# Performance work log

Hardware: AMD Instinct MI355X
Metric: run time of the kernel (lower is better)

## Reference

```python
import jax, jax.numpy as jnp
import numpy as np

EPS_SINK = 0.01   # SinkhornDistance eps
N_ITERS = 20      # fixed iteration count (original: max 100 with host-side early exit)
BN_EPS = 1e-5


def _conv(x, w, b):
    # NCHW 3x3 (or 1x1) conv, SAME padding
    y = jax.lax.conv_general_dilated(x, w, (1, 1), 'SAME',
                                     dimension_numbers=('NCHW', 'OIHW', 'NCHW'))
    return y + b[None, :, None, None]


def _bn_train(x, gamma, beta):
    # BatchNorm2d in training mode: batch statistics over (N,H,W)
    m = jnp.mean(x, axis=(0, 2, 3), keepdims=True)
    v = jnp.var(x, axis=(0, 2, 3), keepdims=True)
    return gamma[None, :, None, None] * (x - m) * jax.lax.rsqrt(v + BN_EPS) + beta[None, :, None, None]


def _calc_mean_std(f, eps=1e-5):
    m = jnp.mean(f, axis=(2, 3), keepdims=True)
    s = jnp.sqrt(jnp.var(f, axis=(2, 3), keepdims=True) + eps)
    return m, s


def _sinkhorn_pi(x, y, eps):
    # x: [b, n, d] content points, y: [b, m, d] style points. Cosine-distance cost.
    xn = x / jnp.linalg.norm(x, axis=-1, keepdims=True)
    yn = y / jnp.linalg.norm(y, axis=-1, keepdims=True)
    C = 1.0 - jnp.einsum('bnd,bmd->bnm', xn, yn)          # [b, n, m]
    b, n, m = C.shape
    log_mu = jnp.log(jnp.full((b, n), 1.0 / n) + 1e-8)
    log_nu = jnp.log(jnp.full((b, m), 1.0 / m) + 1e-8)

    def Mmat(u, v):
        # (-C + u_i + v_j) / eps
        return (-C + u[..., None] + v[..., None, :]) / eps

    def step(carry, _):
        u, v = carry
        u = eps * (log_mu - jax.scipy.special.logsumexp(Mmat(u, v), axis=-1)) + u
        v = eps * (log_nu - jax.scipy.special.logsumexp(Mmat(u, v), axis=-2)) + v
        return (u, v), None

    (u, v), _ = jax.lax.scan(step, (jnp.zeros((b, n)), jnp.zeros((b, m))), None, length=N_ITERS)
    return jnp.exp(Mmat(u, v))                             # transport plan pi


def setup_inputs() -> dict:
    key = jax.random.key(0)
    ks = jax.random.split(key, 16)
    bs, dim, h, w = 4, 512, 32, 32
    s = 0.05
    return {
        'content_feat': jax.random.normal(ks[0], (bs, dim, h, w), jnp.float32),
        'style_feat':   jax.random.normal(ks[1], (bs, dim, h, w), jnp.float32),
        # alpha_predictor (version 1): conv(1024->256,3x3) ReLU BN, conv(256->256,3x3) ReLU BN, conv(256->512,3x3)
        'w1': jax.random.normal(ks[2], (256, 1024, 3, 3), jnp.float32) * s,
        'b1': jnp.zeros((256,), jnp.float32),
        'g1': jnp.ones((256,), jnp.float32),
        'be1': jnp.zeros((256,), jnp.float32),
        'w2': jax.random.normal(ks[3], (256, 256, 3, 3), jnp.float32) * s,
        'b2': jnp.zeros((256,), jnp.float32),
        'g2': jnp.ones((256,), jnp.float32),
        'be2': jnp.zeros((256,), jnp.float32),
        'w3': jax.random.normal(ks[4], (512, 256, 3, 3), jnp.float32) * s,
        'b3': jnp.zeros((512,), jnp.float32),
        # stand-in decoder head: 3x3 conv 512->3 (decoder is an external injected module)
        'dec_w': jax.random.normal(ks[5], (3, 512, 3, 3), jnp.float32) * s,
        'dec_b': jnp.zeros((3,), jnp.float32),
    }


def reference(content_feat, style_feat, w1, b1, g1, be1, w2, b2, g2, be2, w3, b3, dec_w, dec_b):
    bs, dim, h, w = content_feat.shape
    cf = content_feat.reshape(bs, dim, h * w).transpose(0, 2, 1)   # [b, hw, d]
    sf = style_feat.reshape(bs, dim, h * w).transpose(0, 2, 1)
    pi = _sinkhorn_pi(cf, sf, EPS_SINK) * (h * w)                  # style_assign: pi * h * w
    t = jnp.einsum('bnm,bmd->bnd', pi, sf).transpose(0, 2, 1).reshape(bs, dim, h, w)
    cm, cs = _calc_mean_std(content_feat)
    c_normed = (content_feat - cm) / cs
    a = _bn_train(jax.nn.relu(_conv(jnp.concatenate([t, content_feat], axis=1), w1, b1)), g1, be1)
    a = _bn_train(jax.nn.relu(_conv(a, w2, b2)), g2, be2)
    alpha = _conv(a, w3, b3)
    t = alpha * c_normed + t
    g_t = _conv(t, dec_w, dec_b)
    return g_t
```

## Files before the change

### kernel.cpp

```cpp
#include <hip/hip_runtime.h>

typedef unsigned short u16;
typedef unsigned int u32;
typedef float f32x4 __attribute__((ext_vector_type(4)));
typedef short bf16x8 __attribute__((ext_vector_type(8)));

#define DEV static __device__ __forceinline__

DEV float bf2f(u16 u){ union{float f; u32 i;} x; x.i = ((u32)u) << 16; return x.f; }
DEV u16 f2bf(float f){ union{float f; u32 i;} x; x.f = f; u32 u = x.i;
  return (u16)((u + 0x7fffu + ((u >> 16) & 1u)) >> 16); }
DEV u16 f2h(float f){ _Float16 h = (_Float16)f; u16 u; __builtin_memcpy(&u, &h, 2); return u; }
DEV float h2f(u16 u){ _Float16 h; __builtin_memcpy(&h, &u, 2); return (float)h; }
DEV uint4 pack8(const u16* s){ uint4 v;
  v.x = (u32)s[0] | ((u32)s[1]<<16); v.y = (u32)s[2] | ((u32)s[3]<<16);
  v.z = (u32)s[4] | ((u32)s[5]<<16); v.w = (u32)s[6] | ((u32)s[7]<<16); return v; }
DEV f32x4 mfma16(bf16x8 a, bf16x8 b, f32x4 c){
  return __builtin_amdgcn_mfma_f32_16x16x32_bf16(a, b, c, 0, 0, 0);
}
DEV bf16x8 ldfrag(const u16* p){ return *(const bf16x8*)p; }

constexpr float SCL = 144.269504088896341f;
constexpr float LOG2MU = -9.99998522680257f;

constexpr size_t MB = 1ull << 20;
constexpr size_t OFF_G    = 0;
constexpr size_t OFF_GT   = 8*MB;
constexpr size_t OFF_U    = 16*MB;
constexpr size_t OFF_V    = OFF_U   + (16<<10);
constexpr size_t OFF_INC  = OFF_V   + (16<<10);
constexpr size_t OFF_INS  = OFF_INC + (16<<10);
constexpr size_t OFF_CNM  = OFF_INS + (16<<10);
constexpr size_t OFF_CNIS = OFF_CNM + (8<<10);
constexpr size_t OFF_BNS  = OFF_CNIS+ (8<<10);
constexpr size_t OFF_PNP  = OFF_BNS + (4<<10);
constexpr size_t OFF_CFH  = 17*MB;
constexpr size_t OFF_CFL  = 21*MB;
constexpr size_t OFF_SFH  = 25*MB;
constexpr size_t OFF_SFL  = 29*MB;
constexpr size_t OFF_SNB  = 33*MB;
constexpr size_t OFF_TN   = 37*MB;
constexpr size_t OFF_TCP  = 45*MB;
constexpr size_t OFF_W1P  = 53*MB;
constexpr size_t OFF_W2P  = OFF_W1P + 9*256*1024*2;
constexpr size_t OFF_W3P  = OFF_W2P + 9*256*256*2;
constexpr size_t OFF_WDP  = OFF_W3P + 9*512*256*2;
constexpr size_t OFF_PIP  = 62*MB;
constexpr size_t OFF_Z1  = 17*MB;
constexpr size_t OFF_A1P = 25*MB;
constexpr size_t OFF_Z2  = 27*MB;
constexpr size_t OFF_A2P = 35*MB;
constexpr size_t OFF_T2P = 17*MB;

DEV void pack_one(const float* __restrict__ w, u16* __restrict__ wp, int CO, int CI, int o){
  int e = o & 7;
  int lane = (o >> 3) & 63;
  int t2 = o >> 9;
  int tap = t2 % 9;
  int r3 = t2 / 9;
  int NCK = CI >> 5;
  int ck = r3 % NCK;
  int g  = r3 / NCK;
  int co = g*16 + (lane & 15);
  int ci = ck*32 + ((lane >> 4) & 3)*8 + e;
  wp[o] = f2bf(w[(size_t)(co*CI + ci)*9 + tap]);
}

constexpr int NW1 = 9*256*1024, NW2 = 9*256*256, NW3 = 9*512*256, NWD = 9*16*512;
__global__ void pack_all_k(const float* __restrict__ w1, const float* __restrict__ w2,
                           const float* __restrict__ w3, const float* __restrict__ wd,
                           u16* __restrict__ w1p, u16* __restrict__ w2p,
                           u16* __restrict__ w3p, u16* __restrict__ wdp){
  int o = blockIdx.x*256 + threadIdx.x;
  if (o < NW1){ pack_one(w1, w1p, 256, 1024, o); return; }
  o -= NW1;
  if (o < NW2){ pack_one(w2, w2p, 256, 256, o); return; }
  o -= NW2;
  if (o < NW3){ pack_one(w3, w3p, 512, 256, o); return; }
  o -= NW3;
  if (o < NWD){
    int ci = o & 511; int r = o >> 9; int co = r & 15; int tap = r >> 4;
    wdp[o] = f2bf((co < 3) ? wd[(size_t)(co*512 + ci)*9 + tap] : 0.f);
  }
}

__global__ void pix_part_k(const float* __restrict__ cf, const float* __restrict__ sf,
                           float* __restrict__ part){
  int src = blockIdx.z;
  const float* in = src ? sf : cf;
  int p = blockIdx.x*256 + threadIdx.x;
  int b = p >> 10, pp = p & 1023;
  int d0 = blockIdx.y*64;
  const float* base = in + ((size_t)(b*512 + d0))*1024 + pp;
  float s = 0.f;
  #pragma unroll 8
  for (int d = 0; d < 64; ++d){ float x = base[(size_t)d*1024]; s += x*x; }
  part[((size_t)(src*8 + blockIdx.y))*4096 + p] = s;
}

__global__ void pix_fin_k(const float* __restrict__ part, float* __restrict__ inc,
                          float* __restrict__ ins){
  int i = blockIdx.x*256 + threadIdx.x;
  int src = i >> 12, p = i & 4095;
  const float* pp = part + (size_t)src*8*4096 + p;
  float s = 0.f;
  #pragma unroll
  for (int j = 0; j < 8; ++j) s += pp[j*4096];
  (src ? ins : inc)[p] = rsqrtf(s);
}

__global__ void chan_stats_k(const float* __restrict__ cf, float* __restrict__ cnm,
                             float* __restrict__ cnis){
  int bd = blockIdx.x;
  float4 v = ((const float4*)(cf + (size_t)bd*1024))[threadIdx.x];
  float s = v.x+v.y+v.z+v.w;
  float q = v.x*v.x+v.y*v.y+v.z*v.z+v.w*v.w;
  #pragma unroll
  for (int m = 32; m >= 1; m >>= 1){ s += __shfl_xor(s, m, 64); q += __shfl_xor(q, m, 64); }
  __shared__ float ls[4], lq[4];
  int w = threadIdx.x >> 6;
  if ((threadIdx.x & 63) == 0){ ls[w] = s; lq[w] = q; }
  __syncthreads();
  if (threadIdx.x == 0){
    float S = ls[0]+ls[1]+ls[2]+ls[3], Q = lq[0]+lq[1]+lq[2]+lq[3];
    float mean = S * (1.f/1024.f);
    float var  = Q * (1.f/1024.f) - mean*mean;
    cnm[bd] = mean; cnis[bd] = rsqrtf(var + 1e-5f);
  }
}

__global__ void tsplit_k(const float* __restrict__ src, const float* __restrict__ invn,
                         u16* __restrict__ hi, u16* __restrict__ lo,
                         u16* __restrict__ aux, int is_style){
  __shared__ float tile[64][65];
  int b = blockIdx.z, p0 = blockIdx.x*64, d0 = blockIdx.y*64;
  int r = threadIdx.x >> 2, c0 = (threadIdx.x & 3) * 16;
  const float* sp = src + ((size_t)(b*512 + d0 + r))*1024 + p0 + c0;
  float v[16];
  #pragma unroll
  for (int e = 0; e < 4; ++e){
    float4 t4 = ((const float4*)sp)[e];
    v[e*4+0]=t4.x; v[e*4+1]=t4.y; v[e*4+2]=t4.z; v[e*4+3]=t4.w;
  }
  #pragma unroll
  for (int j = 0; j < 16; ++j) tile[r][c0+j] = v[j];
  if (is_style){
    u16 t16[16];
    #pragma unroll
    for (int j = 0; j < 16; ++j) t16[j] = f2bf(v[j]);
    uint4* ap = (uint4*)(aux + ((size_t)(b*512 + d0 + r))*1024 + p0 + c0);
    ap[0] = pack8(t16); ap[1] = pack8(t16+8);
  }
  __syncthreads();
  int pr = r, dc0 = c0;
  float inv = invn[(b<<10) + p0 + pr];
  u16 h16[16], l16[16], t16[16];
  #pragma unroll
  for (int j = 0; j < 16; ++j){
    float x = tile[dc0+j][pr];
    t16[j] = f2bf(x);
    float xn = x * inv;
    u16 h = f2bf(xn);
    h16[j] = h;
    l16[j] = f2bf(xn - bf2f(h));
  }
  size_t orow = (size_t)((b<<10) + p0 + pr);
  uint4* hp = (uint4*)(hi + orow*512 + d0 + dc0);
  uint4* lp = (uint4*)(lo + orow*512 + d0 + dc0);
  hp[0] = pack8(h16); hp[1] = pack8(h16+8);
  lp[0] = pack8(l16); lp[1] = pack8(l16+8);
  if (!is_style){
    int D = d0 + dc0;
    size_t off = ((size_t)(16 + (D>>5))*4096 + orow)*32 + (D&31);
    *(uint4*)(aux + off)     = pack8(t16);
    *(uint4*)(aux + off + 8) = pack8(t16+8);
  }
}

__global__ __launch_bounds__(256) void cgemm_k(const u16* __restrict__ cfh, const u16* __restrict__ cfl,
        const u16* __restrict__ sfh, const u16* __restrict__ sfl,
        u16* __restrict__ G){
  __shared__ __align__(16) u16 Ah[128*40], Al[128*40], Bh[128*40], Bl[128*40];
  int b = blockIdx.z;
  size_t abase = ((size_t)((b<<10) + blockIdx.x*128))*512;
  size_t bbase = ((size_t)((b<<10) + blockIdx.y*128))*512;
  int lane = threadIdx.x & 63, wid = threadIdx.x >> 6;
  int wm = (wid >> 1)*64, wn = (wid & 1)*64;
  int fr = lane & 15, qd = lane >> 4;
  int sr = threadIdx.x >> 1, sc = (threadIdx.x & 1)*16;
  f32x4 acc[4][4] = {};
  for (int kk = 0; kk < 512; kk += 32){
    size_t g0 = (size_t)sr*512 + kk + sc;
    *(uint4*)&Ah[sr*40+sc]   = *(const uint4*)(cfh + abase + g0);
    *(uint4*)&Ah[sr*40+sc+8] = *(const uint4*)(cfh + abase + g0 + 8);
    *(uint4*)&Al[sr*40+sc]   = *(const uint4*)(cfl + abase + g0);
    *(uint4*)&Al[sr*40+sc+8] = *(const uint4*)(cfl + abase + g0 + 8);
    *(uint4*)&Bh[sr*40+sc]   = *(const uint4*)(sfh + bbase + g0);
    *(uint4*)&Bh[sr*40+sc+8] = *(const uint4*)(sfh + bbase + g0 + 8);
    *(uint4*)&Bl[sr*40+sc]   = *(const uint4*)(sfl + bbase + g0);
    *(uint4*)&Bl[sr*40+sc+8] = *(const uint4*)(sfl + bbase + g0 + 8);
    __syncthreads();
    bf16x8 bhf[4], blf[4];
    #pragma unroll
    for (int ni = 0; ni < 4; ++ni){
      bhf[ni] = ldfrag(&Bh[(wn + ni*16 + fr)*40 + qd*8]);
      blf[ni] = ldfrag(&Bl[(wn + ni*16 + fr)*40 + qd*8]);
    }
    #pragma unroll
    for (int mi = 0; mi < 4; ++mi){
      bf16x8 ah = ldfrag(&Ah[(wm + mi*16 + fr)*40 + qd*8]);
      bf16x8 al = ldfrag(&Al[(wm + mi*16 + fr)*40 + qd*8]);
      #pragma unroll
      for (int ni = 0; ni < 4; ++ni){
        acc[mi][ni] = mfma16(ah, bhf[ni], acc[mi][ni]);
        acc[mi][ni] = mfma16(ah, blf[ni], acc[mi][ni]);
        acc[mi][ni] = mfma16(al, bhf[ni], acc[mi][ni]);
      }
    }
    __syncthreads();
  }
  size_t gb = ((size_t)b) << 20;
  #pragma unroll
  for (int mi = 0; mi < 4; ++mi)
    #pragma unroll
    for (int ni = 0; ni < 4; ++ni)
      #pragma unroll
      for (int rg = 0; rg < 4; ++rg){
        int ig = blockIdx.x*128 + wm + mi*16 + qd*4 + rg;
        int jg = blockIdx.y*128 + wn + ni*16 + fr;
        G[gb + (size_t)ig*1024 + jg] = f2h((acc[mi][ni][rg] - 1.f) * SCL);
      }
}

__global__ __launch_bounds__(256) void trans_k(const u16* __restrict__ G, u16* __restrict__ Gt){
  __shared__ u16 T[64][66];
  int b = blockIdx.z, x0 = blockIdx.x*64, y0 = blockIdx.y*64;
  int t = threadIdx.x;
  int r = t >> 2, c0 = (t & 3)*16;
  const u16* src = G + (((size_t)((b<<10) + y0 + r)) << 10) + x0 + c0;
  uint4 v0 = ((const uint4*)src)[0], v1 = ((const uint4*)src)[1];
  u32 w[8] = {v0.x,v0.y,v0.z,v0.w,v1.x,v1.y,v1.z,v1.w};
  #pragma unroll
  for (int k = 0; k < 8; ++k){
    T[r][c0 + 2*k]     = (u16)(w[k] & 0xffffu);
    T[r][c0 + 2*k + 1] = (u16)(w[k] >> 16);
  }
  __syncthreads();
  u16 o[16];
  #pragma unroll
  for (int k = 0; k < 16; ++k) o[k] = T[c0 + k][r];
  u16* dst = Gt + (((size_t)((b<<10) + x0 + r)) << 10) + y0 + c0;
  ((uint4*)dst)[0] = pack8(o);
  ((uint4*)dst)[1] = pack8(o + 8);
}

__global__ void lse_k(const u16* __restrict__ M, const float* __restrict__ addv,
                      float* __restrict__ outv){
  int row = blockIdx.x*4 + (threadIdx.x >> 6);
  int lane = threadIdx.x & 63;
  int b = row >> 10;
  const uint4* r4 = (const uint4*)(M + ((size_t)row << 10));
  const float4* a4 = (const float4*)(addv + ((size_t)b << 10));
  float x[16]; float mx = -3.0e38f;
  #pragma unroll
  for (int e = 0; e < 2; ++e){
    uint4 g = r4[lane + 64*e];
    float4 a0 = a4[2*(lane + 64*e)];
    float4 a1 = a4[2*(lane + 64*e) + 1];
    u32 w[4] = {g.x, g.y, g.z, g.w};
    float av[8] = {a0.x,a0.y,a0.z,a0.w,a1.x,a1.y,a1.z,a1.w};
    #pragma unroll
    for (int i = 0; i < 8; ++i){
      u16 hv = (u16)((i & 1) ? (w[i>>1] >> 16) : (w[i>>1] & 0xffffu));
      float t = h2f(hv) + av[i];
      x[e*8+i] = t;
      mx = fmaxf(mx, t);
    }
  }
  #pragma unroll
  for (int m = 32; m >= 1; m >>= 1) mx = fmaxf(mx, __shfl_xor(mx, m, 64));
  float s = 0.f;
  #pragma unroll
  for (int i = 0; i < 16; ++i) s += exp2f(x[i] - mx);
  #pragma unroll
  for (int m = 32; m >= 1; m >>= 1) s += __shfl_xor(s, m, 64);
  if (lane == 0) outv[row] = LOG2MU - (mx + log2f(s));
}

__global__ void pi_k(const u16* __restrict__ G, const float* __restrict__ U,
                     const float* __restrict__ V, u16* __restrict__ pip){
  int row = blockIdx.x, b = row >> 10, t = threadIdx.x;
  float ur = U[row] + 10.f;
  uint2 g = ((const uint2*)(G + ((size_t)row << 10)))[t];
  float4 vv = ((const float4*)(V + ((size_t)b << 10)))[t];
  u16 o[4];
  o[0] = f2bf(exp2f(h2f((u16)(g.x & 0xffffu)) + vv.x + ur));
  o[1] = f2bf(exp2f(h2f((u16)(g.x >> 16))     + vv.y + ur));
  o[2] = f2bf(exp2f(h2f((u16)(g.y & 0xffffu)) + vv.z + ur));
  o[3] = f2bf(exp2f(h2f((u16)(g.y >> 16))     + vv.w + ur));
  uint2 pk; pk.x = (u32)o[0] | ((u32)o[1]<<16); pk.y = (u32)o[2] | ((u32)o[3]<<16);
  ((uint2*)(pip + ((size_t)row << 10)))[t] = pk;
}

__global__ __launch_bounds__(256) void tgemm_k(const u16* __restrict__ pip,
        const u16* __restrict__ snb, float* __restrict__ tn, u16* __restrict__ tcp){
  __shared__ __align__(16) u16 As[64*40], Bs[128*40];
  int b = blockIdx.z, p0 = blockIdx.x*64, d0 = blockIdx.y*128;
  int tid = threadIdx.x, lane = tid & 63, wid = tid >> 6;
  int wm = (wid >> 1)*32, wn = (wid & 1)*64;
  int fr = lane & 15, qd = lane >> 4;
  int a_r = tid >> 2, a_c = (tid & 3)*8;
  int b_r = tid >> 1, b_c = (tid & 1)*16;
  const u16* Arow = pip + (((size_t)((b<<10) + p0 + a_r)) << 10) + a_c;
  const u16* Brow = snb + (((size_t)(b*512 + d0 + b_r)) << 10) + b_c;
  uint4 pa, pb0, pb1;
  auto issue = [&](int kk){
    pa = *(const uint4*)(Arow + kk);
    const uint4* bp = (const uint4*)(Brow + kk);
    pb0 = bp[0]; pb1 = bp[1];
  };
  f32x4 acc[2][4] = {};
  issue(0);
  for (int kk = 0; kk < 1024; kk += 32){
    *(uint4*)&As[a_r*40 + a_c] = pa;
    *(uint4*)&Bs[b_r*40 + b_c] = pb0;
    *(uint4*)&Bs[b_r*40 + b_c + 8] = pb1;
    __syncthreads();
    if (kk + 32 < 1024) issue(kk + 32);
    bf16x8 bfr[4];
    #pragma unroll
    for (int ni = 0; ni < 4; ++ni) bfr[ni] = ldfrag(&Bs[(wn + ni*16 + fr)*40 + qd*8]);
    #pragma unroll
    for (int mi = 0; mi < 2; ++mi){
      bf16x8 afr = ldfrag(&As[(wm + mi*16 + fr)*40 + qd*8]);
      #pragma unroll
      for (int ni = 0; ni < 4; ++ni) acc[mi][ni] = mfma16(afr, bfr[ni], acc[mi][ni]);
    }
    __syncthreads();
  }
  #pragma unroll
  for (int mi = 0; mi < 2; ++mi)
    #pragma unroll
    for (int ni = 0; ni < 4; ++ni)
      #pragma unroll
      for (int rg = 0; rg < 4; ++rg){
        int p = p0 + wm + mi*16 + qd*4 + rg;
        int d = d0 + wn + ni*16 + fr;
        float vout = acc[mi][ni][rg];
        size_t ro = (size_t)((b<<10) + p);
        tn[ro*512 + d] = vout;
        tcp[((size_t)(d>>5)*4096 + ro)*32 + (d&31)] = f2bf(vout);
      }
}

template<int CI, int CO, int KSPLIT, int MODE>
__global__ __launch_bounds__(256) void conv_k(const u16* __restrict__ inp, const u16* __restrict__ wpk,
        const float* __restrict__ bias, float* __restrict__ fout, u16* __restrict__ bout,
        const u16* __restrict__ tcp, const float* __restrict__ cnm, const float* __restrict__ cnis,
        const float* __restrict__ tn){
  constexpr int NCK_TOT = CI/32, NCK = NCK_TOT/KSPLIT;
  __shared__ __align__(16) u16 As[128*40];
  int b = blockIdx.z & 3, ks = blockIdx.z >> 2;
  int c0 = blockIdx.y*64;
  int r0 = blockIdx.x*2;
  int tid = threadIdx.x, lane = tid & 63, wid = tid >> 6;
  int wm = (wid >> 1)*32, wn = (wid & 1)*32;
  int fr = lane & 15, qd = lane >> 4;
  int ck0 = ks*NCK;
  int hrow = tid >> 1;
  int ah = (tid & 1)*16;
  int gy = r0 - 1 + (hrow >> 5);
  bool a_ok = ((unsigned)gy < 32u);
  size_t arow = (size_t)(b<<10) + (r0-1)*32 + hrow;
  uint4 pa0 = {0,0,0,0}, pa1 = {0,0,0,0};
  auto issueA = [&](int ck){
    if (a_ok){
      const uint4* s = (const uint4*)(inp + ((size_t)(ck0+ck)*4096 + arow)*32 + ah);
      pa0 = s[0]; pa1 = s[1];
    }
  };
  int g0 = (c0 + wn) >> 4;
  const u16* wb0 = wpk + ((size_t)(g0    )*NCK_TOT + ck0)*9*512 + lane*8;
  const u16* wb1 = wpk + ((size_t)(g0 + 1)*NCK_TOT + ck0)*9*512 + lane*8;

  f32x4 acc[2][2] = {};
  issueA(0);
  for (int ck = 0; ck < NCK; ++ck){
    *(uint4*)&As[hrow*40 + ah]     = pa0;
    *(uint4*)&As[hrow*40 + ah + 8] = pa1;
    __syncthreads();
    if (ck + 1 < NCK) issueA(ck + 1);
    #pragma unroll
    for (int tap = 0; tap < 9; ++tap){
      const int dy = tap/3 - 1, dx = tap%3 - 1;
      bf16x8 bf0 = ldfrag(wb0 + (size_t)(ck*9 + tap)*512);
      bf16x8 bf1 = ldfrag(wb1 + (size_t)(ck*9 + tap)*512);
      #pragma unroll
      for (int mi = 0; mi < 2; ++mi){
        int p0w = wm + mi*16;
        int pcol = (p0w & 31) + fr + dx;
        int lr = (p0w >> 5) + dy + 1;
        bool okc = (unsigned)pcol < 32u;
        bf16x8 af = ldfrag(&As[(lr*32 + (okc ? pcol : 0))*40 + qd*8]);
        if (!okc) af = bf16x8(0);
        acc[mi][0] = mfma16(af, bf0, acc[mi][0]);
        acc[mi][1] = mfma16(af, bf1, acc[mi][1]);
      }
    }
    __syncthreads();
  }
  #pragma unroll
  for (int mi = 0; mi < 2; ++mi)
    #pragma unroll
    for (int ni = 0; ni < 2; ++ni)
      #pragma unroll
      for (int rg = 0; rg < 4; ++rg){
        int pp = blockIdx.x*64 + wm + mi*16 + qd*4 + rg;
        int cc = c0 + wn + ni*16 + fr;
        float v = acc[mi][ni][rg];
        size_t ro = (size_t)((b<<10) + pp);
        if (MODE == 0){
          fout[(size_t)ks*4096*CO + ro*CO + cc] = v;
        } else {
          float alpha = v + bias[cc];
          float cn = (bf2f(tcp[((size_t)(16 + (cc>>5))*4096 + ro)*32 + (cc&31)])
                      - cnm[(b<<9) + cc]) * cnis[(b<<9) + cc];
          bout[((size_t)(cc>>5)*4096 + ro)*32 + (cc&31)] = f2bf(alpha*cn + tn[ro*512 + cc]);
        }
      }
}

__global__ __launch_bounds__(256) void dec_k(const u16* __restrict__ t2p, const u16* __restrict__ wdp,
                                             const float* __restrict__ db, float* __restrict__ out){
  __shared__ float wlds[3*4608];
  int tid = threadIdx.x;
  for (int k = tid; k < 3*4608; k += 256){
    int c = k / 4608, rem = k - c*4608;
    int tap = rem >> 9, ci = rem & 511;
    wlds[k] = bf2f(wdp[(size_t)(tap*16 + c)*512 + ci]);
  }
  __syncthreads();
  int b = blockIdx.x >> 6;
  int p = ((blockIdx.x & 63) << 4) + (tid >> 4);
  int sub = tid & 15;
  int py = p >> 5, px = p & 31;
  float a0 = 0.f, a1 = 0.f, a2 = 0.f;
  for (int tap = 0; tap < 9; ++tap){
    int sy = py + tap/3 - 1, sx = px + tap%3 - 1;
    if (((unsigned)sy < 32u) && ((unsigned)sx < 32u)){
      size_t row = (size_t)((b<<10) + (sy<<5) + sx);
      const float* w0 = wlds + tap*512;
      #pragma unroll
      for (int j = 0; j < 4; ++j){
        int ci0 = j*128 + sub*8;
        uint4 v = *(const uint4*)(t2p + ((size_t)(ci0>>5)*4096 + row)*32 + (ci0&31));
        u32 ww[4] = {v.x, v.y, v.z, v.w};
        #pragma unroll
        for (int e = 0; e < 8; ++e){
          float x = bf2f((u16)((e & 1) ? (ww[e>>1] >> 16) : (ww[e>>1] & 0xffffu)));
          a0 += x * w0[ci0 + e];
          a1 += x * w0[4608 + ci0 + e];
          a2 += x * w0[9216 + ci0 + e];
        }
      }
    }
  }
  #pragma unroll
  for (int m = 8; m >= 1; m >>= 1){
    a0 += __shfl_xor(a0, m, 64);
    a1 += __shfl_xor(a1, m, 64);
    a2 += __shfl_xor(a2, m, 64);
  }
  if (sub == 0){
    out[((size_t)(b*3 + 0) << 10) + p] = a0 + db[0];
    out[((size_t)(b*3 + 1) << 10) + p] = a1 + db[1];
    out[((size_t)(b*3 + 2) << 10) + p] = a2 + db[2];
  }
}

__global__ void bn_stats_k(const float* __restrict__ z, const float* __restrict__ bias,
                           float* __restrict__ sums){
  int c = blockIdx.x*64 + (threadIdx.x & 63);
  int w = threadIdx.x >> 6;
  int rbase = blockIdx.y*512 + w*128;
  float bi = bias[c];
  float s = 0.f, q = 0.f;
  for (int i = 0; i < 128; ++i){
    size_t ro = (size_t)(rbase + i)*256 + c;
    float x = fmaxf(z[ro] + z[4096*256 + ro] + bi, 0.f);
    s += x; q += x*x;
  }
  __shared__ float ls[4][64], lq[4][64];
  ls[w][threadIdx.x & 63] = s; lq[w][threadIdx.x & 63] = q;
  __syncthreads();
  if (threadIdx.x < 64){
    float S = ls[0][threadIdx.x]+ls[1][threadIdx.x]+ls[2][threadIdx.x]+ls[3][threadIdx.x];
    float Q = lq[0][threadIdx.x]+lq[1][threadIdx.x]+lq[2][threadIdx.x]+lq[3][threadIdx.x];
    atomicAdd(&sums[blockIdx.x*64 + threadIdx.x], S);
    atomicAdd(&sums[256 + blockIdx.x*64 + threadIdx.x], Q);
  }
}

__global__ void bn_apply_k(const float* __restrict__ z, const float* __restrict__ bias,
                           const float* __restrict__ sums, const float* __restrict__ gamma,
                           const float* __restrict__ beta, u16* __restrict__ ap){
  int idx = blockIdx.x*256 + threadIdx.x;
  float4 va = ((const float4*)z)[idx];
  float4 vb = ((const float4*)(z + 4096*256))[idx];
  int row = idx >> 6;
  int cc0 = (idx << 2) & 255;
  float e[4] = {va.x+vb.x, va.y+vb.y, va.z+vb.z, va.w+vb.w};
  u16 o[4];
  #pragma unroll
  for (int k = 0; k < 4; ++k){
    int c = cc0 + k;
    float mean = sums[c] * (1.f/4096.f);
    float var  = sums[256 + c] * (1.f/4096.f) - mean*mean;
    float sc = gamma[c] * rsqrtf(var + 1e-5f);
    float sh = beta[c] - mean*sc;
    float x = fmaxf(e[k] + bias[c], 0.f);
    o[k] = f2bf(x*sc + sh);
  }
  uint2 pk; pk.x = (u32)o[0] | ((u32)o[1]<<16); pk.y = (u32)o[2] | ((u32)o[3]<<16);
  *(uint2*)(ap + ((size_t)(cc0>>5)*4096 + row)*32 + (cc0&31)) = pk;
}

extern "C" void kernel_launch(void* const* d_in, const int* in_sizes, int n_in,
                              void* d_out, int out_size, void* d_ws, size_t ws_size,
                              hipStream_t stream){
  const float* cf  = (const float*)d_in[0];
  const float* sf  = (const float*)d_in[1];
  const float* w1  = (const float*)d_in[2];
  const float* b1  = (const float*)d_in[3];
  const float* g1  = (const float*)d_in[4];
  const float* be1 = (const float*)d_in[5];
  const float* w2  = (const float*)d_in[6];
  const float* b2  = (const float*)d_in[7];
  const float* g2  = (const float*)d_in[8];
  const float* be2 = (const float*)d_in[9];
  const float* w3  = (const float*)d_in[10];
  const float* b3  = (const float*)d_in[11];
  const float* dw  = (const float*)d_in[12];
  const float* db  = (const float*)d_in[13];

  char* ws = (char*)d_ws;
  u16* G    = (u16*)(ws + OFF_G);
  u16* Gt   = (u16*)(ws + OFF_GT);
  float* U    = (float*)(ws + OFF_U);
  float* V    = (float*)(ws + OFF_V);
  float* inc  = (float*)(ws + OFF_INC);
  float* ins  = (float*)(ws + OFF_INS);
  float* cnm  = (float*)(ws + OFF_CNM);
  float* cnis = (float*)(ws + OFF_CNIS);
  float* bns1 = (float*)(ws + OFF_BNS);
  float* bns2 = bns1 + 512;
  float* pnp  = (float*)(ws + OFF_PNP);
  u16* cfh = (u16*)(ws + OFF_CFH);
  u16* cfl = (u16*)(ws + OFF_CFL);
  u16* sfh = (u16*)(ws + OFF_SFH);
  u16* sfl = (u16*)(ws + OFF_SFL);
  u16* snb = (u16*)(ws + OFF_SNB);
  float* tn  = (float*)(ws + OFF_TN);
  u16* tcp = (u16*)(ws + OFF_TCP);
  u16* w1p = (u16*)(ws + OFF_W1P);
  u16* w2p = (u16*)(ws + OFF_W2P);
  u16* w3p = (u16*)(ws + OFF_W3P);
  u16* wdp = (u16*)(ws + OFF_WDP);
  u16* pip = (u16*)(ws + OFF_PIP);
  float* z1  = (float*)(ws + OFF_Z1);
  u16*   a1p = (u16*)(ws + OFF_A1P);
  float* z2  = (float*)(ws + OFF_Z2);
  u16*   a2p = (u16*)(ws + OFF_A2P);
  u16*   t2p = (u16*)(ws + OFF_T2P);

  hipMemsetAsync(ws + OFF_U, 0, 32 << 10, stream);
  hipMemsetAsync(ws + OFF_BNS, 0, 4 << 10, stream);

  pack_all_k<<<(NW1+NW2+NW3+NWD + 255)/256, 256, 0, stream>>>(
      w1, w2, w3, dw, w1p, w2p, w3p, wdp);

  pix_part_k<<<dim3(16, 8, 2), 256, 0, stream>>>(cf, sf, pnp);
  pix_fin_k<<<32, 256, 0, stream>>>(pnp, inc, ins);
  chan_stats_k<<<2048, 256, 0, stream>>>(cf, cnm, cnis);
  tsplit_k<<<dim3(16, 8, 4), 256, 0, stream>>>(cf, inc, cfh, cfl, tcp, 0);
  tsplit_k<<<dim3(16, 8, 4), 256, 0, stream>>>(sf, ins, sfh, sfl, snb, 1);

  cgemm_k<<<dim3(8, 8, 4), 256, 0, stream>>>(cfh, cfl, sfh, sfl, G);
  trans_k<<<dim3(16, 16, 4), 256, 0, stream>>>(G, Gt);

  for (int it = 0; it < 20; ++it){
    lse_k<<<1024, 256, 0, stream>>>(G,  V, U);
    lse_k<<<1024, 256, 0, stream>>>(Gt, U, V);
  }

  pi_k<<<4096, 256, 0, stream>>>(G, U, V, pip);
  tgemm_k<<<dim3(16, 4, 4), 256, 0, stream>>>(pip, snb, tn, tcp);

  conv_k<1024, 256, 2, 0><<<dim3(16, 4, 8), 256, 0, stream>>>(
      tcp, w1p, nullptr, z1, nullptr, nullptr, nullptr, nullptr, nullptr);
  bn_stats_k<<<dim3(4, 8), 256, 0, stream>>>(z1, b1, bns1);
  bn_apply_k<<<1024, 256, 0, stream>>>(z1, b1, bns1, g1, be1, a1p);

  conv_k<256, 256, 2, 0><<<dim3(16, 4, 8), 256, 0, stream>>>(
      a1p, w2p, nullptr, z2, nullptr, nullptr, nullptr, nullptr, nullptr);
  bn_stats_k<<<dim3(4, 8), 256, 0, stream>>>(z2, b2, bns2);
  bn_apply_k<<<1024, 256, 0, stream>>>(z2, b2, bns2, g2, be2, a2p);

  conv_k<256, 512, 1, 1><<<dim3(16, 8, 4), 256, 0, stream>>>(
      a2p, w3p, b3, nullptr, t2p, tcp, cnm, cnis, tn);

  dec_k<<<256, 256, 0, stream>>>(t2p, wdp, db, (float*)d_out);

  (void)in_sizes; (void)n_in; (void)out_size; (void)ws_size;
}
```

Before: 435.9 us.

## Restructure preprocessing: LDS-staged weight packing, merged stats kernels, prefetched cgemm loads

Weight packing now stages each 16-output by 32-input-channel slice in shared memory so global reads are coalesced instead of strided gathers. The per-pixel norm partials and channel stats are merged into one kernel, and the norm finalisation is folded into tsplit, which removes two launches. The two memsets become one. cgemm now loads the next k-tile into registers while MFMA work runs on the current tile, at the cost of extra registers.

```diff
diff --git a/kernel.cpp b/kernel.cpp
--- a/kernel.cpp
+++ b/kernel.cpp
@@ -52,84 +52,77 @@
 constexpr size_t OFF_A2P = 35*MB;
 constexpr size_t OFF_T2P = 17*MB;
 
-DEV void pack_one(const float* __restrict__ w, u16* __restrict__ wp, int CO, int CI, int o){
-  int e = o & 7;
-  int lane = (o >> 3) & 63;
-  int t2 = o >> 9;
-  int tap = t2 % 9;
-  int r3 = t2 / 9;
-  int NCK = CI >> 5;
-  int ck = r3 % NCK;
-  int g  = r3 / NCK;
-  int co = g*16 + (lane & 15);
-  int ci = ck*32 + ((lane >> 4) & 3)*8 + e;
-  wp[o] = f2bf(w[(size_t)(co*CI + ci)*9 + tap]);
-}
-
-constexpr int NW1 = 9*256*1024, NW2 = 9*256*256, NW3 = 9*512*256, NWD = 9*16*512;
 __global__ void pack_all_k(const float* __restrict__ w1, const float* __restrict__ w2,
                            const float* __restrict__ w3, const float* __restrict__ wd,
                            u16* __restrict__ w1p, u16* __restrict__ w2p,
                            u16* __restrict__ w3p, u16* __restrict__ wdp){
-  int o = blockIdx.x*256 + threadIdx.x;
-  if (o < NW1){ pack_one(w1, w1p, 256, 1024, o); return; }
-  o -= NW1;
-  if (o < NW2){ pack_one(w2, w2p, 256, 256, o); return; }
-  o -= NW2;
-  if (o < NW3){ pack_one(w3, w3p, 512, 256, o); return; }
-  o -= NW3;
-  if (o < NWD){
+  int blk = blockIdx.x;
+  const float* w; u16* wp; int CI, NCK, rel;
+  if (blk < 512){ w = w1; wp = w1p; CI = 1024; NCK = 32; rel = blk; }
+  else if (blk < 640){ w = w2; wp = w2p; CI = 256; NCK = 8; rel = blk - 512; }
+  else if (blk < 896){ w = w3; wp = w3p; CI = 256; NCK = 8; rel = blk - 640; }
+  else {
+    int o = (blk - 896)*256 + threadIdx.x;
     int ci = o & 511; int r = o >> 9; int co = r & 15; int tap = r >> 4;
     wdp[o] = f2bf((co < 3) ? wd[(size_t)(co*512 + ci)*9 + tap] : 0.f);
-  }
-}
-
-__global__ void pix_part_k(const float* __restrict__ cf, const float* __restrict__ sf,
-                           float* __restrict__ part){
-  int src = blockIdx.z;
+    return;
+  }
+  int g = rel / NCK, ck = rel % NCK;
+  __shared__ float L[16*288];
+  const float* base = w + ((size_t)(g*16)*CI + ck*32)*9;
+  #pragma unroll
+  for (int i = 0; i < 18; ++i){
+    int idx = i*256 + threadIdx.x;
+    int row = idx / 288, col = idx - row*288;
+    L[row*288 + col] = base[(size_t)row*CI*9 + col];
+  }
+  __syncthreads();
+  u16* dst = wp + ((size_t)(g*NCK + ck)*9)*512;
+  #pragma unroll
+  for (int i = 0; i < 18; ++i){
+    int j = i*256 + threadIdx.x;
+    int tap = j >> 9, r = j & 511, lane = r >> 3, e = r & 7;
+    int co = lane & 15, cil = ((lane >> 4) & 3)*8 + e;
+    dst[j] = f2bf(L[co*288 + cil*9 + tap]);
+  }
+}
+
+__global__ void stats_k(const float* __restrict__ cf, const float* __restrict__ sf,
+                        float* __restrict__ cnm, float* __restrict__ cnis,
+                        float* __restrict__ part){
+  int blk = blockIdx.x;
+  if (blk < 2048){
+    int bd = blk;
+    float4 v = ((const float4*)(cf + (size_t)bd*1024))[threadIdx.x];
+    float s = v.x+v.y+v.z+v.w;
+    float q = v.x*v.x+v.y*v.y+v.z*v.z+v.w*v.w;
+    #pragma unroll
+    for (int m = 32; m >= 1; m >>= 1){ s += __shfl_xor(s, m, 64); q += __shfl_xor(q, m, 64); }
+    __shared__ float ls[4], lq[4];
+    int w = threadIdx.x >> 6;
+    if ((threadIdx.x & 63) == 0){ ls[w] = s; lq[w] = q; }
+    __syncthreads();
+    if (threadIdx.x == 0){
+      float S = ls[0]+ls[1]+ls[2]+ls[3], Q = lq[0]+lq[1]+lq[2]+lq[3];
+      float mean = S * (1.f/1024.f);
+      float var  = Q * (1.f/1024.f) - mean*mean;
+      cnm[bd] = mean; cnis[bd] = rsqrtf(var + 1e-5f);
+    }
+    return;
+  }
+  int rel = blk - 2048;
+  int x = rel & 15, y = (rel >> 4) & 7, src = rel >> 7;
   const float* in = src ? sf : cf;
-  int p = blockIdx.x*256 + threadIdx.x;
+  int p = x*256 + threadIdx.x;
   int b = p >> 10, pp = p & 1023;
-  int d0 = blockIdx.y*64;
-  const float* base = in + ((size_t)(b*512 + d0))*1024 + pp;
+  const float* base = in + ((size_t)(b*512 + y*64))*1024 + pp;
   float s = 0.f;
   #pragma unroll 8
-  for (int d = 0; d < 64; ++d){ float x = base[(size_t)d*1024]; s += x*x; }
-  part[((size_t)(src*8 + blockIdx.y))*4096 + p] = s;
-}
-
-__global__ void pix_fin_k(const float* __restrict__ part, float* __restrict__ inc,
-                          float* __restrict__ ins){
-  int i = blockIdx.x*256 + threadIdx.x;
-  int src = i >> 12, p = i & 4095;
-  const float* pp = part + (size_t)src*8*4096 + p;
-  float s = 0.f;
-  #pragma unroll
-  for (int j = 0; j < 8; ++j) s += pp[j*4096];
-  (src ? ins : inc)[p] = rsqrtf(s);
-}
-
-__global__ void chan_stats_k(const float* __restrict__ cf, float* __restrict__ cnm,
-                             float* __restrict__ cnis){
-  int bd = blockIdx.x;
-  float4 v = ((const float4*)(cf + (size_t)bd*1024))[threadIdx.x];
-  float s = v.x+v.y+v.z+v.w;
-  float q = v.x*v.x+v.y*v.y+v.z*v.z+v.w*v.w;
-  #pragma unroll
-  for (int m = 32; m >= 1; m >>= 1){ s += __shfl_xor(s, m, 64); q += __shfl_xor(q, m, 64); }
-  __shared__ float ls[4], lq[4];
-  int w = threadIdx.x >> 6;
-  if ((threadIdx.x & 63) == 0){ ls[w] = s; lq[w] = q; }
-  __syncthreads();
-  if (threadIdx.x == 0){
-    float S = ls[0]+ls[1]+ls[2]+ls[3], Q = lq[0]+lq[1]+lq[2]+lq[3];
-    float mean = S * (1.f/1024.f);
-    float var  = Q * (1.f/1024.f) - mean*mean;
-    cnm[bd] = mean; cnis[bd] = rsqrtf(var + 1e-5f);
-  }
-}
-
-__global__ void tsplit_k(const float* __restrict__ src, const float* __restrict__ invn,
+  for (int d = 0; d < 64; ++d){ float xx = base[(size_t)d*1024]; s += xx*xx; }
+  part[((size_t)(src*8 + y))*4096 + p] = s;
+}
+
+__global__ void tsplit_k(const float* __restrict__ src, const float* __restrict__ pnp,
                          u16* __restrict__ hi, u16* __restrict__ lo,
                          u16* __restrict__ aux, int is_style){
   __shared__ float tile[64][65];
@@ -153,7 +146,14 @@
   }
   __syncthreads();
   int pr = r, dc0 = c0;
-  float inv = invn[(b<<10) + p0 + pr];
+  float inv;
+  {
+    const float* pp = pnp + (size_t)(is_style ? 8*4096 : 0) + ((b<<10) + p0 + pr);
+    float s = 0.f;
+    #pragma unroll
+    for (int j = 0; j < 8; ++j) s += pp[j*4096];
+    inv = rsqrtf(s);
+  }
   u16 h16[16], l16[16], t16[16];
   #pragma unroll
   for (int j = 0; j < 16; ++j){
@@ -188,18 +188,23 @@
   int wm = (wid >> 1)*64, wn = (wid & 1)*64;
   int fr = lane & 15, qd = lane >> 4;
   int sr = threadIdx.x >> 1, sc = (threadIdx.x & 1)*16;
+  uint4 p[8];
+  auto issue = [&](int kk){
+    size_t g0 = (size_t)sr*512 + kk + sc;
+    p[0] = *(const uint4*)(cfh + abase + g0); p[1] = *(const uint4*)(cfh + abase + g0 + 8);
+    p[2] = *(const uint4*)(cfl + abase + g0); p[3] = *(const uint4*)(cfl + abase + g0 + 8);
+    p[4] = *(const uint4*)(sfh + bbase + g0); p[5] = *(const uint4*)(sfh + bbase + g0 + 8);
+    p[6] = *(const uint4*)(sfl + bbase + g0); p[7] = *(const uint4*)(sfl + bbase + g0 + 8);
+  };
   f32x4 acc[4][4] = {};
+  issue(0);
   for (int kk = 0; kk < 512; kk += 32){
-    size_t g0 = (size_t)sr*512 + kk + sc;
-    *(uint4*)&Ah[sr*40+sc]   = *(const uint4*)(cfh + abase + g0);
-    *(uint4*)&Ah[sr*40+sc+8] = *(const uint4*)(cfh + abase + g0 + 8);
-    *(uint4*)&Al[sr*40+sc]   = *(const uint4*)(cfl + abase + g0);
-    *(uint4*)&Al[sr*40+sc+8] = *(const uint4*)(cfl + abase + g0 + 8);
-    *(uint4*)&Bh[sr*40+sc]   = *(const uint4*)(sfh + bbase + g0);
-    *(uint4*)&Bh[sr*40+sc+8] = *(const uint4*)(sfh + bbase + g0 + 8);
-    *(uint4*)&Bl[sr*40+sc]   = *(const uint4*)(sfl + bbase + g0);
-    *(uint4*)&Bl[sr*40+sc+8] = *(const uint4*)(sfl + bbase + g0 + 8);
+    *(uint4*)&Ah[sr*40+sc]   = p[0]; *(uint4*)&Ah[sr*40+sc+8] = p[1];
+    *(uint4*)&Al[sr*40+sc]   = p[2]; *(uint4*)&Al[sr*40+sc+8] = p[3];
+    *(uint4*)&Bh[sr*40+sc]   = p[4]; *(uint4*)&Bh[sr*40+sc+8] = p[5];
+    *(uint4*)&Bl[sr*40+sc]   = p[6]; *(uint4*)&Bl[sr*40+sc+8] = p[7];
     __syncthreads();
+    if (kk + 32 < 512) issue(kk + 32);
     bf16x8 bhf[4], blf[4];
     #pragma unroll
     for (int ni = 0; ni < 4; ++ni){
@@ -548,8 +553,6 @@
   u16* Gt   = (u16*)(ws + OFF_GT);
   float* U    = (float*)(ws + OFF_U);
   float* V    = (float*)(ws + OFF_V);
-  float* inc  = (float*)(ws + OFF_INC);
-  float* ins  = (float*)(ws + OFF_INS);
   float* cnm  = (float*)(ws + OFF_CNM);
   float* cnis = (float*)(ws + OFF_CNIS);
   float* bns1 = (float*)(ws + OFF_BNS);
@@ -573,17 +576,13 @@
   u16*   a2p = (u16*)(ws + OFF_A2P);
   u16*   t2p = (u16*)(ws + OFF_T2P);
 
-  hipMemsetAsync(ws + OFF_U, 0, 32 << 10, stream);
-  hipMemsetAsync(ws + OFF_BNS, 0, 4 << 10, stream);
-
-  pack_all_k<<<(NW1+NW2+NW3+NWD + 255)/256, 256, 0, stream>>>(
-      w1, w2, w3, dw, w1p, w2p, w3p, wdp);
-
-  pix_part_k<<<dim3(16, 8, 2), 256, 0, stream>>>(cf, sf, pnp);
-  pix_fin_k<<<32, 256, 0, stream>>>(pnp, inc, ins);
-  chan_stats_k<<<2048, 256, 0, stream>>>(cf, cnm, cnis);
-  tsplit_k<<<dim3(16, 8, 4), 256, 0, stream>>>(cf, inc, cfh, cfl, tcp, 0);
-  tsplit_k<<<dim3(16, 8, 4), 256, 0, stream>>>(sf, ins, sfh, sfl, snb, 1);
+  hipMemsetAsync(ws + OFF_U, 0, 84 << 10, stream);
+
+  pack_all_k<<<1184, 256, 0, stream>>>(w1, w2, w3, dw, w1p, w2p, w3p, wdp);
+
+  stats_k<<<2304, 256, 0, stream>>>(cf, sf, cnm, cnis, pnp);
+  tsplit_k<<<dim3(16, 8, 4), 256, 0, stream>>>(cf, pnp, cfh, cfl, tcp, 0);
+  tsplit_k<<<dim3(16, 8, 4), 256, 0, stream>>>(sf, pnp, sfh, sfl, snb, 1);
 
   cgemm_k<<<dim3(8, 8, 4), 256, 0, stream>>>(cfh, cfl, sfh, sfl, G);
   trans_k<<<dim3(16, 16, 4), 256, 0, stream>>>(G, Gt);
```

Measured after the change: 444.3 us. About the same (+1.9%).
